# Performance work log

Hardware: AMD Instinct MI355X
Metric: run time of the kernel (lower is better)

Reference implementation:

```python
import jax, jax.numpy as jnp
import numpy as np

CK = 16          # ck_size
REP50 = 50       # extra_feature.repeat(1, 50)
BN_EPS = 1e-5
SLOPE = 0.01     # LeakyReLU default slope

def leaky(x):
    return jnp.where(x >= 0, x, SLOPE * x)

def bn(x):
    # BatchNorm1d(affine=False, track_running_stats=False): per-call batch stats
    m = jnp.mean(x, axis=0, keepdims=True)
    v = jnp.var(x, axis=0, keepdims=True)
    return (x - m) * jax.lax.rsqrt(v + BN_EPS)

def rev_within(x, lengths):
    # reverse each sequence within its valid length, keep padding in place
    B, T, _ = x.shape
    t = jnp.arange(T)[None, :]
    idx = jnp.where(t < lengths[:, None], lengths[:, None] - 1 - t, t)
    return jnp.take_along_axis(x, idx[:, :, None], axis=1)

def lstm(x, lengths, Wih, Whh, bih, bhh):
    # masked unidirectional LSTM; padded steps output zeros (pad_packed behavior)
    B, T, D = x.shape
    H = Whh.shape[1]
    xg = jnp.einsum('btd,gd->btg', x, Wih) + bih + bhh             # [B,T,4H]
    mask = (jnp.arange(T)[None, :] < lengths[:, None])[..., None]  # [B,T,1]
    def step(carry, inp):
        h, c = carry
        g, m = inp
        g = g + h @ Whh.T
        i, f, gg, o = jnp.split(g, 4, axis=-1)  # torch gate order i,f,g,o
        c_new = jax.nn.sigmoid(f) * c + jax.nn.sigmoid(i) * jnp.tanh(gg)
        h_new = jax.nn.sigmoid(o) * jnp.tanh(c_new)
        h = jnp.where(m, h_new, h)
        c = jnp.where(m, c_new, c)
        return (h, c), h_new * m
    init = (jnp.zeros((B, H), x.dtype), jnp.zeros((B, H), x.dtype))
    _, outs = jax.lax.scan(step, init, (xg.transpose(1, 0, 2), mask.transpose(1, 0, 2)))
    return outs.transpose(1, 0, 2)  # [B,T,H]

def att_var(inputs, lengths, s1_w, s1_b, s2_w):
    # NOTE: faithful to source softmax_by_length, which (due to the original
    # code) normalizes the *raw* masked logits linearly; exp() is discarded.
    B, T, D = inputs.shape
    utt = leaky(bn(inputs.reshape(-1, D) @ s1_w.T + s1_b))
    alpha = (utt @ s2_w.T).reshape(B, T)
    m = (jnp.arange(T)[None, :] < lengths[:, None]).astype(alpha.dtype)
    am = alpha * m
    alpha_ = am / (jnp.sum(am, axis=1, keepdims=True) + 1e-9)
    return jnp.einsum('bt,btd->bd', alpha_, inputs)

def item_att(x, y):
    # x: [D], y: [N, D] -> [N, 3D+1]
    xb = jnp.broadcast_to(x, y.shape)
    dist = jnp.linalg.norm(xb - y, axis=-1, keepdims=True)
    return jnp.concatenate([xb, y, dist, xb * y], axis=-1)


def setup_inputs() -> dict:
    key = jax.random.key(0)
    ks = jax.random.split(key, 30)
    D, T, B = 1024, 128, 256
    Ne, Nc, P = 64, 128, 50
    Hh = D // 2
    f32 = jnp.float32
    def rn(k, shape, s=0.05):
        return jax.random.normal(k, shape, f32) * s
    inp = {}
    inp['word_encode'] = jax.random.normal(ks[0], (B, T, D), f32)
    inp['pos_encode'] = jax.random.normal(ks[1], (Ne, Nc // CK, P), f32)
    inp['dis_encode'] = jax.random.normal(ks[2], (Ne, Nc, P), f32)
    sl = jax.random.randint(ks[3], (B,), T // 2, T + 1)
    inp['sen_lengths'] = sl.at[0].set(T)
    inp['label3'] = jax.random.randint(ks[4], (Ne, 3), -1, Nc)
    inp['emo_idx'] = jnp.arange(Ne)
    inp['cau_idx'] = jnp.arange(Ne, Ne + Nc)
    # BiLSTM params (torch layout: [4H, in])
    inp['Wih_f'] = rn(ks[5], (4 * Hh, D)); inp['Whh_f'] = rn(ks[6], (4 * Hh, Hh))
    inp['bih_f'] = rn(ks[7], (4 * Hh,));  inp['bhh_f'] = rn(ks[8], (4 * Hh,))
    inp['Wih_b'] = rn(ks[9], (4 * Hh, D)); inp['Whh_b'] = rn(ks[10], (4 * Hh, Hh))
    inp['bih_b'] = rn(ks[11], (4 * Hh,)); inp['bhh_b'] = rn(ks[12], (4 * Hh,))
    # attention / projection params
    inp['s1_w'] = rn(ks[13], (D, D)); inp['s1_b'] = rn(ks[14], (D,))
    inp['s2_w'] = rn(ks[15], (1, D))
    inp['W2_w'] = rn(ks[16], (D, 3 * D + 1 + P)); inp['W2_b'] = rn(ks[17], (D,))
    inp['Wo_w'] = rn(ks[18], (2, D)); inp['Wo_b'] = rn(ks[19], (2,))
    inp['W3_w'] = rn(ks[20], (D, 3 * D + 51 + P)); inp['W3_b'] = rn(ks[21], (D,))
    inp['cls_w'] = rn(ks[22], (2, D)); inp['cls_b'] = rn(ks[23], (2,))
    return inp


def reference(word_encode, pos_encode, dis_encode,
              Wih_f, Whh_f, bih_f, bhh_f, Wih_b, Whh_b, bih_b, bhh_b,
              s1_w, s1_b, s2_w, W2_w, W2_b, Wo_w, Wo_b, W3_w, W3_b, cls_w, cls_b,
              sen_lengths, label3, emo_idx, cau_idx):
    lengths = sen_lengths
    out_f = lstm(word_encode, lengths, Wih_f, Whh_f, bih_f, bhh_f)
    out_b = rev_within(lstm(rev_within(word_encode, lengths), lengths,
                            Wih_b, Whh_b, bih_b, bhh_b), lengths)
    Hseq = jnp.concatenate([out_f, out_b], axis=-1)          # [B,T,D]
    U = att_var(Hseq, lengths, s1_w, s1_b, s2_w)             # [B,D]
    text_emo = U[emo_idx]                                    # [Ne,D]
    text_cau = U[cau_idx]                                    # [Nc,D]
    Nc, D = text_cau.shape
    Ne = text_emo.shape[0]
    cau_chunks = text_cau.reshape(Nc // CK, CK, D)           # [Nck,CK,D]

    # ground-truth cause labels per emotion (label3 -> binary over cau utts)
    valid = (label3 >= 0)
    safe = jnp.where(valid, label3, 0)
    L = jnp.zeros((Ne, Nc), U.dtype).at[jnp.arange(Ne)[:, None], safe].max(valid.astype(U.dtype))

    def per_emo(emo, pos_j, dis_j):
        # phase-2: chunk-level attention + classification
        sc = jax.nn.softmax(jnp.einsum('d,ncd->nc', emo, cau_chunks), axis=1)
        chunkEmb = jnp.einsum('nc,ncd->nd', sc, cau_chunks)          # [Nck,D]
        delta = jnp.concatenate([item_att(emo, chunkEmb), pos_j], -1)
        hidden = leaky(bn(delta @ W2_w.T + W2_b))
        out2 = jax.nn.log_softmax(hidden @ Wo_w.T + Wo_b, axis=-1)   # [Nck,2]
        # phase-3: utterance-level with chunk prediction as extra feature
        extra = jnp.repeat(jnp.argmax(out2, axis=-1).astype(emo.dtype), CK)[:, None]
        delta_ = jnp.concatenate([item_att(emo, text_cau), dis_j,
                                  jnp.tile(extra, (1, REP50))], -1)
        h = leaky(bn(delta_ @ W3_w.T + W3_b))
        p = jax.nn.log_softmax(h @ cls_w.T + cls_b, axis=-1)         # [Nc,2]
        return out2, p

    phase2, p3 = jax.vmap(per_emo)(text_emo, pos_encode, dis_encode)
    return phase2, p3, L
```

## Files before the change

kernel.cpp:

```cpp
#include <hip/hip_runtime.h>
#include <math.h>

#define DD    1024
#define TT    128
#define BB    256
#define NE    64
#define NCC   128
#define PPP   50
#define NCK   8
#define HH    512
#define G4    2048
#define NROWS 32768
#define K3PAD 3200
#define CHUNK 8

#define F_HSEQ  0ull
#define F_XG    33554432ull
#define F_WIH   41943040ull
#define F_WHH   46137344ull
#define F_S1    48234496ull
#define F_W2    49283072ull
#define F_W3    52559872ull
#define F_BIASC 56885248ull
#define F_HST   56889344ull
#define F_CST   57413632ull
#define F_CS    57675776ull
#define F_CSQ   57676800ull
#define F_BNM   57677824ull
#define F_BNI   57678848ull
#define F_ALPHA 57679872ull
#define F_U     57712640ull
#define F_H2    57974784ull
#define F_BN2M  58499072ull
#define F_BN2I  58564608ull
#define F_EXTRA 58630144ull
#define F_BN3M  58631168ull
#define F_BN3I  58696704ull

#define F_D2    F_HSEQ
#define F_CHE   (F_HSEQ + 26214400ull)
#define F_D3    F_HSEQ
#define F_H3    F_XG

typedef short s8v __attribute__((ext_vector_type(8)));
typedef float f4v __attribute__((ext_vector_type(4)));

__device__ __forceinline__ float leakyf(float x) { return x >= 0.f ? x : 0.01f * x; }
__device__ __forceinline__ float sigmf(float x)  { return 1.f / (1.f + __expf(-x)); }

__device__ __forceinline__ float blk_sum(float v, float* s4) {
  for (int o = 32; o > 0; o >>= 1) v += __shfl_down(v, o);
  __syncthreads();
  if ((threadIdx.x & 63) == 0) s4[threadIdx.x >> 6] = v;
  __syncthreads();
  return s4[0] + s4[1] + s4[2] + s4[3];
}

__device__ __forceinline__ void cvt2(float x0, float x1, unsigned& hi, unsigned& lo) {
  unsigned b0 = __float_as_uint(x0), b1 = __float_as_uint(x1);
  hi = (b0 >> 16) | (b1 & 0xffff0000u);
  float h0 = __uint_as_float(b0 & 0xffff0000u);
  float h1 = __uint_as_float(b1 & 0xffff0000u);
  unsigned l0 = __float_as_uint(x0 - h0);
  unsigned l1 = __float_as_uint(x1 - h1);
  lo = (l0 >> 16) | (l1 & 0xffff0000u);
}

__global__ __launch_bounds__(256) void k_cvt(const float* __restrict__ src,
                                             unsigned short* __restrict__ hi,
                                             unsigned short* __restrict__ lo,
                                             int Ks, int Kd) {
  int n = blockIdx.x;
  for (int k = threadIdx.x; k < Kd; k += 256) {
    float v = (k < Ks) ? src[(size_t)n * Ks + k] : 0.f;
    unsigned b = __float_as_uint(v);
    float h = __uint_as_float(b & 0xffff0000u);
    hi[(size_t)n * Kd + k] = (unsigned short)(b >> 16);
    lo[(size_t)n * Kd + k] = (unsigned short)(__float_as_uint(v - h) >> 16);
  }
}

__global__ __launch_bounds__(256) void k_biasc(const float* __restrict__ bf1, const float* __restrict__ bf2,
                                               const float* __restrict__ bb1, const float* __restrict__ bb2,
                                               float* __restrict__ out) {
  int i = blockIdx.x * 256 + threadIdx.x;
  if (i < G4) out[i] = bf1[i] + bf2[i];
  else        out[i] = bb1[i - G4] + bb2[i - G4];
}

template <int MODE>
__global__ __launch_bounds__(256, 2) void k_mf(
    const float* __restrict__ A,
    const unsigned short* __restrict__ Ahi, const unsigned short* __restrict__ Alo,
    const unsigned short* __restrict__ Bhi, const unsigned short* __restrict__ Blo,
    const float* __restrict__ bias, float* __restrict__ C, int M, int N, int K,
    const int* __restrict__ lens, int c,
    const float* __restrict__ bnm, const float* __restrict__ bni,
    const float* __restrict__ s2w, float* __restrict__ cs,
    float* __restrict__ csq, float* __restrict__ alpha) {
  __shared__ unsigned short Ah[128][40];
  __shared__ unsigned short Al[128][40];
  __shared__ unsigned short Bh[128][40];
  __shared__ unsigned short Bl[128][40];
  const int tid = threadIdx.x;
  const int m0 = blockIdx.x * 128;
  const int n0 = blockIdx.y * 128;
  const int dir = (MODE == 3) ? blockIdx.z : 0;

  const int sr = tid >> 1;
  const int sh = tid & 1;
  const float* arow = nullptr;
  const unsigned short* ahrow = nullptr;
  const unsigned short* alrow = nullptr;
  if (MODE == 3) {
    int tl = m0 >> 8;
    int b = (m0 & 255) + sr;
    int t = c * CHUNK + tl;
    int len = lens[b];
    int r = (dir == 0) ? t : ((t < len) ? (len - 1 - t) : t);
    arow = A + ((size_t)b * TT + r) * DD;
  } else if (MODE == 0) {
    arow = A + (size_t)(m0 + sr) * K;
  } else {
    ahrow = Ahi + (size_t)(m0 + sr) * K;
    alrow = Alo + (size_t)(m0 + sr) * K;
  }
  const unsigned short* bhrow = Bhi + ((size_t)dir * N + n0 + sr) * K;
  const unsigned short* blrow = Blo + ((size_t)dir * N + n0 + sr) * K;

  const int wave = tid >> 6, lane = tid & 63;
  const int wm = wave & 1, wn = wave >> 1;
  const int quad = lane >> 4, l15 = lane & 15;

  f4v acc[4][4];
#pragma unroll
  for (int i = 0; i < 4; ++i)
#pragma unroll
    for (int j = 0; j < 4; ++j) acc[i][j] = (f4v){0.f, 0.f, 0.f, 0.f};

#pragma unroll 1
  for (int k0 = 0; k0 < K; k0 += 32) {
    __syncthreads();
    if (MODE == 1 || MODE == 2) {
      const uint4* ph = (const uint4*)(ahrow + k0 + sh * 16);
      uint4* dh = (uint4*)&Ah[sr][sh * 16];
      dh[0] = ph[0]; dh[1] = ph[1];
      const uint4* pl = (const uint4*)(alrow + k0 + sh * 16);
      uint4* dl = (uint4*)&Al[sr][sh * 16];
      dl[0] = pl[0]; dl[1] = pl[1];
    } else {
      const float4* pa = (const float4*)(arow + k0 + sh * 16);
      float4 v0 = pa[0], v1 = pa[1], v2 = pa[2], v3 = pa[3];
      unsigned h[8], l[8];
      cvt2(v0.x, v0.y, h[0], l[0]); cvt2(v0.z, v0.w, h[1], l[1]);
      cvt2(v1.x, v1.y, h[2], l[2]); cvt2(v1.z, v1.w, h[3], l[3]);
      cvt2(v2.x, v2.y, h[4], l[4]); cvt2(v2.z, v2.w, h[5], l[5]);
      cvt2(v3.x, v3.y, h[6], l[6]); cvt2(v3.z, v3.w, h[7], l[7]);
      uint4* dh = (uint4*)&Ah[sr][sh * 16];
      dh[0] = make_uint4(h[0], h[1], h[2], h[3]);
      dh[1] = make_uint4(h[4], h[5], h[6], h[7]);
      uint4* dl = (uint4*)&Al[sr][sh * 16];
      dl[0] = make_uint4(l[0], l[1], l[2], l[3]);
      dl[1] = make_uint4(l[4], l[5], l[6], l[7]);
    }
    {
      const uint4* pbh = (const uint4*)(bhrow + k0 + sh * 16);
      uint4* dbh = (uint4*)&Bh[sr][sh * 16];
      dbh[0] = pbh[0]; dbh[1] = pbh[1];
      const uint4* pbl = (const uint4*)(blrow + k0 + sh * 16);
      uint4* dbl = (uint4*)&Bl[sr][sh * 16];
      dbl[0] = pbl[0]; dbl[1] = pbl[1];
    }
    __syncthreads();
    s8v ah[4], al[4], bh[4], bl[4];
#pragma unroll
    for (int mi = 0; mi < 4; ++mi) {
      ah[mi] = *(const s8v*)&Ah[wm * 64 + mi * 16 + l15][quad * 8];
      al[mi] = *(const s8v*)&Al[wm * 64 + mi * 16 + l15][quad * 8];
    }
#pragma unroll
    for (int ni = 0; ni < 4; ++ni) {
      bh[ni] = *(const s8v*)&Bh[wn * 64 + ni * 16 + l15][quad * 8];
      bl[ni] = *(const s8v*)&Bl[wn * 64 + ni * 16 + l15][quad * 8];
    }
#pragma unroll
    for (int mi = 0; mi < 4; ++mi)
#pragma unroll
      for (int ni = 0; ni < 4; ++ni) {
        acc[mi][ni] = __builtin_amdgcn_mfma_f32_16x16x32_bf16(ah[mi], bh[ni], acc[mi][ni], 0, 0, 0);
        acc[mi][ni] = __builtin_amdgcn_mfma_f32_16x16x32_bf16(al[mi], bh[ni], acc[mi][ni], 0, 0, 0);
        acc[mi][ni] = __builtin_amdgcn_mfma_f32_16x16x32_bf16(ah[mi], bl[ni], acc[mi][ni], 0, 0, 0);
      }
  }

  const int rb = wm * 64;
  if (MODE == 0 || MODE == 3) {
    float* Cb;
    const float* bp = bias;
    if (MODE == 3) {
      int tl = m0 >> 8;
      Cb = C + (((size_t)dir * CHUNK + tl) * 256 + (m0 & 255)) * (size_t)N;
      bp = bias + (size_t)dir * N;
    } else {
      Cb = C + (size_t)m0 * N;
    }
#pragma unroll
    for (int mi = 0; mi < 4; ++mi)
#pragma unroll
      for (int ni = 0; ni < 4; ++ni) {
        int col = n0 + wn * 64 + ni * 16 + l15;
        float bv = bp[col];
#pragma unroll
        for (int r = 0; r < 4; ++r) {
          int row = rb + mi * 16 + quad * 4 + r;
          Cb[(size_t)row * N + col] = acc[mi][ni][r] + bv;
        }
      }
  } else if (MODE == 1) {
#pragma unroll
    for (int ni = 0; ni < 4; ++ni) {
      int col = n0 + wn * 64 + ni * 16 + l15;
      float bv = bias[col];
      float s = 0.f, q = 0.f;
#pragma unroll
      for (int mi = 0; mi < 4; ++mi)
#pragma unroll
        for (int r = 0; r < 4; ++r) {
          float z = acc[mi][ni][r] + bv;
          s += z;
          q += z * z;
        }
      s += __shfl_xor(s, 16); s += __shfl_xor(s, 32);
      q += __shfl_xor(q, 16); q += __shfl_xor(q, 32);
      if (quad == 0) {
        atomicAdd(&cs[col], s);
        atomicAdd(&csq[col], q);
      }
    }
  } else {
#pragma unroll
    for (int mi = 0; mi < 4; ++mi) {
      float rv[4] = {0.f, 0.f, 0.f, 0.f};
#pragma unroll
      for (int ni = 0; ni < 4; ++ni) {
        int col = n0 + wn * 64 + ni * 16 + l15;
        float bv = bias[col], mc = bnm[col], ic = bni[col], wc = s2w[col];
#pragma unroll
        for (int r = 0; r < 4; ++r) {
          float z = acc[mi][ni][r] + bv;
          rv[r] += leakyf((z - mc) * ic) * wc;
        }
      }
#pragma unroll
      for (int r = 0; r < 4; ++r) {
        float v = rv[r];
        v += __shfl_xor(v, 1); v += __shfl_xor(v, 2);
        v += __shfl_xor(v, 4); v += __shfl_xor(v, 8);
        if (l15 == 0) atomicAdd(&alpha[m0 + rb + mi * 16 + quad * 4 + r], v);
      }
    }
  }
}

__global__ __launch_bounds__(256, 2) void k_rec(
    const unsigned short* __restrict__ Bhi, const unsigned short* __restrict__ Blo,
    const float* __restrict__ XG, const int* __restrict__ lens,
    const float* __restrict__ Hcur, float* __restrict__ Hnext,
    float* __restrict__ Cst,
    unsigned short* __restrict__ Hhi, unsigned short* __restrict__ Hlo, int t) {
  __shared__ unsigned short Ah[64][40];
  __shared__ unsigned short Al[64][40];
  __shared__ unsigned short Bh[64][40];
  __shared__ unsigned short Bl[64][40];
  const int tid = threadIdx.x;
  const int b0 = blockIdx.x * 64;
  const int j0 = blockIdx.y * 16;
  const int dir = blockIdx.z;
  const int tl = t & (CHUNK - 1);
  const int srow = tid >> 2;
  const int skq = (tid & 3) * 8;
  const int bg = srow >> 4, bjj = srow & 15;
  const float* arow = Hcur + ((size_t)dir * BB + b0 + srow) * HH;
  const unsigned short* bhrow = Bhi + ((size_t)dir * G4 + bg * HH + j0 + bjj) * HH;
  const unsigned short* blrow = Blo + ((size_t)dir * G4 + bg * HH + j0 + bjj) * HH;
  const int wave = tid >> 6, lane = tid & 63;
  const int quad = lane >> 4, l15 = lane & 15;

  f4v acc[4];
#pragma unroll
  for (int g = 0; g < 4; ++g) acc[g] = (f4v){0.f, 0.f, 0.f, 0.f};

#pragma unroll 1
  for (int k0 = 0; k0 < HH; k0 += 32) {
    __syncthreads();
    {
      const float4* pa = (const float4*)(arow + k0 + skq);
      float4 v0 = pa[0], v1 = pa[1];
      unsigned h[4], l[4];
      cvt2(v0.x, v0.y, h[0], l[0]); cvt2(v0.z, v0.w, h[1], l[1]);
      cvt2(v1.x, v1.y, h[2], l[2]); cvt2(v1.z, v1.w, h[3], l[3]);
      *(uint4*)&Ah[srow][skq] = make_uint4(h[0], h[1], h[2], h[3]);
      *(uint4*)&Al[srow][skq] = make_uint4(l[0], l[1], l[2], l[3]);
      *(uint4*)&Bh[srow][skq] = *(const uint4*)(bhrow + k0 + skq);
      *(uint4*)&Bl[srow][skq] = *(const uint4*)(blrow + k0 + skq);
    }
    __syncthreads();
    s8v ah = *(const s8v*)&Ah[wave * 16 + l15][quad * 8];
    s8v al = *(const s8v*)&Al[wave * 16 + l15][quad * 8];
#pragma unroll
    for (int g = 0; g < 4; ++g) {
      s8v bh = *(const s8v*)&Bh[g * 16 + l15][quad * 8];
      s8v bl = *(const s8v*)&Bl[g * 16 + l15][quad * 8];
      acc[g] = __builtin_amdgcn_mfma_f32_16x16x32_bf16(ah, bh, acc[g], 0, 0, 0);
      acc[g] = __builtin_amdgcn_mfma_f32_16x16x32_bf16(al, bh, acc[g], 0, 0, 0);
      acc[g] = __builtin_amdgcn_mfma_f32_16x16x32_bf16(ah, bl, acc[g], 0, 0, 0);
    }
  }

  const int j = j0 + l15;
#pragma unroll
  for (int r = 0; r < 4; ++r) {
    int b = b0 + wave * 16 + quad * 4 + r;
    int len = lens[b];
    bool m = t < len;
    size_t xgb = (((size_t)dir * CHUNK + tl) * BB + b) * G4 + j;
    float gi = acc[0][r] + XG[xgb];
    float gf = acc[1][r] + XG[xgb + HH];
    float gg = acc[2][r] + XG[xgb + 2 * HH];
    float go = acc[3][r] + XG[xgb + 3 * HH];
    size_t sidx = ((size_t)dir * BB + b) * HH + j;
    float c_old = Cst[sidx];
    float cn = sigmf(gf) * c_old + sigmf(gi) * tanhf(gg);
    float hn = sigmf(go) * tanhf(cn);
    if (m) {
      Cst[sidx] = cn;
      Hnext[sidx] = hn;
      int ro = dir ? (len - 1 - t) : t;
      size_t hidx = ((size_t)b * TT + ro) * DD + dir * HH + j;
      unsigned hb = __float_as_uint(hn);
      Hhi[hidx] = (unsigned short)(hb >> 16);
      Hlo[hidx] = (unsigned short)(__float_as_uint(hn - __uint_as_float(hb & 0xffff0000u)) >> 16);
    } else {
      Hnext[sidx] = Hcur[sidx];
    }
  }
}

__global__ __launch_bounds__(256) void k_bnfinal(const float* __restrict__ cs, const float* __restrict__ csq,
                                                 float* __restrict__ bnm, float* __restrict__ bni, float invN) {
  int i = blockIdx.x * 256 + threadIdx.x;
  if (i < DD) {
    float m = cs[i] * invN;
    float v = csq[i] * invN - m * m;
    bnm[i] = m;
    bni[i] = rsqrtf(v + 1e-5f);
  }
}

__global__ __launch_bounds__(128) void k_asum(float* __restrict__ alpha, const int* __restrict__ lens) {
  int b = blockIdx.x;
  int t = threadIdx.x;
  int len = lens[b];
  float v = (t < len) ? alpha[b * TT + t] : 0.f;
  float s = v;
  for (int o = 32; o > 0; o >>= 1) s += __shfl_down(s, o);
  __shared__ float sw[2];
  if ((t & 63) == 0) sw[t >> 6] = s;
  __syncthreads();
  float S = sw[0] + sw[1] + 1e-9f;
  alpha[b * TT + t] = v / S;
}

__global__ __launch_bounds__(256) void k_U(const unsigned short* __restrict__ Hhi,
                                           const unsigned short* __restrict__ Hlo,
                                           const float* __restrict__ alpha,
                                           float* __restrict__ U) {
  int b = blockIdx.x;
  int tid = threadIdx.x;
  __shared__ float al[TT];
  if (tid < TT) al[tid] = alpha[b * TT + tid];
  __syncthreads();
  float4 s = make_float4(0.f, 0.f, 0.f, 0.f);
  size_t base = (size_t)b * TT * DD + tid * 4;
#pragma unroll 4
  for (int t = 0; t < TT; ++t) {
    float a = al[t];
    ushort4 hv = *(const ushort4*)(Hhi + base + (size_t)t * DD);
    ushort4 lv = *(const ushort4*)(Hlo + base + (size_t)t * DD);
    s.x += a * (__uint_as_float((unsigned)hv.x << 16) + __uint_as_float((unsigned)lv.x << 16));
    s.y += a * (__uint_as_float((unsigned)hv.y << 16) + __uint_as_float((unsigned)lv.y << 16));
    s.z += a * (__uint_as_float((unsigned)hv.z << 16) + __uint_as_float((unsigned)lv.z << 16));
    s.w += a * (__uint_as_float((unsigned)hv.w << 16) + __uint_as_float((unsigned)lv.w << 16));
  }
  *(float4*)(U + (size_t)b * DD + tid * 4) = s;
}

__global__ __launch_bounds__(256) void k_p2a(const float* __restrict__ U,
                                             const int* __restrict__ emoI,
                                             const int* __restrict__ cauI,
                                             float* __restrict__ chunkEmb) {
  int e = blockIdx.x;
  int tid = threadIdx.x;
  __shared__ float emoS[DD];
  __shared__ float sc[NCK][16];
  const float* Ue = U + (size_t)emoI[e] * DD;
  for (int i = tid; i < DD; i += 256) emoS[i] = Ue[i];
  __syncthreads();
  int w = tid >> 6, lane = tid & 63;
  for (int p = w; p < 128; p += 4) {
    const float* y = U + (size_t)cauI[p] * DD;
    float s = 0;
    for (int d = lane; d < DD; d += 64) s += emoS[d] * y[d];
    for (int o = 32; o > 0; o >>= 1) s += __shfl_down(s, o);
    if (lane == 0) sc[p >> 4][p & 15] = s;
  }
  __syncthreads();
  if (tid < NCK) {
    float mx = -1e30f;
    for (int c = 0; c < 16; ++c) mx = fmaxf(mx, sc[tid][c]);
    float sum = 0;
    for (int c = 0; c < 16; ++c) {
      float ev = __expf(sc[tid][c] - mx);
      sc[tid][c] = ev;
      sum += ev;
    }
    float inv = 1.f / sum;
    for (int c = 0; c < 16; ++c) sc[tid][c] *= inv;
  }
  __syncthreads();
  int d = tid * 4;
  for (int nn = 0; nn < NCK; ++nn) {
    float4 s = make_float4(0.f, 0.f, 0.f, 0.f);
    for (int c = 0; c < 16; ++c) {
      float wc = sc[nn][c];
      float4 y = *(const float4*)(U + (size_t)cauI[nn * 16 + c] * DD + d);
      s.x += wc * y.x; s.y += wc * y.y; s.z += wc * y.z; s.w += wc * y.w;
    }
    *(float4*)(chunkEmb + ((size_t)e * NCK + nn) * DD + d) = s;
  }
}

__global__ __launch_bounds__(256) void k_delta2(const float* __restrict__ U,
                                                const int* __restrict__ emoI,
                                                const float* __restrict__ chunkEmb,
                                                const float* __restrict__ pos,
                                                float* __restrict__ delta2) {
  int e = blockIdx.x >> 3, nn = blockIdx.x & 7;
  int tid = threadIdx.x;
  const float* emo = U + (size_t)emoI[e] * DD;
  const float* y = chunkEmb + ((size_t)e * NCK + nn) * DD;
  __shared__ float s4[4];
  float ds = 0;
  for (int d = tid; d < DD; d += 256) {
    float df = emo[d] - y[d];
    ds += df * df;
  }
  float dist = sqrtf(blk_sum(ds, s4));
  float* out = delta2 + ((size_t)e * NCK + nn) * K3PAD;
  for (int c = tid; c < K3PAD; c += 256) {
    float v;
    if (c < 1024) v = emo[c];
    else if (c < 2048) v = y[c - 1024];
    else if (c == 2048) v = dist;
    else if (c < 3073) { int d = c - 2049; v = emo[d] * y[d]; }
    else if (c < 3123) v = pos[((size_t)e * NCK + nn) * PPP + (c - 3073)];
    else v = 0.f;
    out[c] = v;
  }
}

__global__ __launch_bounds__(256) void k_bnstats(const float* __restrict__ X,
                                                 float* __restrict__ bm, float* __restrict__ bi, int R) {
  int gid = blockIdx.x * 256 + threadIdx.x;
  int e = gid >> 10, col = gid & 1023;
  const float* p = X + (size_t)e * R * DD + col;
  float s = 0, s2 = 0;
  for (int r = 0; r < R; ++r) {
    float v = p[(size_t)r * DD];
    s += v;
    s2 += v * v;
  }
  float m = s / R;
  float var = s2 / R - m * m;
  bm[gid] = m;
  bi[gid] = rsqrtf(var + 1e-5f);
}

__global__ __launch_bounds__(256) void k_out2(const float* __restrict__ h2,
                                              const float* __restrict__ bm, const float* __restrict__ bi,
                                              const float* __restrict__ Wo, const float* __restrict__ Wob,
                                              float* __restrict__ out, float* __restrict__ extraf) {
  int e = blockIdx.x >> 3, nn = blockIdx.x & 7;
  int tid = threadIdx.x;
  const float* row = h2 + ((size_t)e * NCK + nn) * DD;
  float l0 = 0, l1 = 0;
  for (int col = tid; col < DD; col += 256) {
    float h = leakyf((row[col] - bm[e * DD + col]) * bi[e * DD + col]);
    l0 += h * Wo[col];
    l1 += h * Wo[DD + col];
  }
  __shared__ float s4[4];
  l0 = blk_sum(l0, s4);
  l1 = blk_sum(l1, s4);
  if (tid == 0) {
    l0 += Wob[0];
    l1 += Wob[1];
    float mx = fmaxf(l0, l1);
    float lse = mx + logf(__expf(l0 - mx) + __expf(l1 - mx));
    out[((size_t)e * NCK + nn) * 2 + 0] = l0 - lse;
    out[((size_t)e * NCK + nn) * 2 + 1] = l1 - lse;
    extraf[e * NCK + nn] = (l1 > l0) ? 1.f : 0.f;
  }
}

__global__ __launch_bounds__(256) void k_delta3(const float* __restrict__ U,
                                                const int* __restrict__ emoI,
                                                const int* __restrict__ cauI,
                                                const float* __restrict__ dis,
                                                const float* __restrict__ extraf,
                                                float* __restrict__ delta3) {
  int e = blockIdx.x >> 7, c = blockIdx.x & 127;
  int tid = threadIdx.x;
  const float* emo = U + (size_t)emoI[e] * DD;
  const float* y = U + (size_t)cauI[c] * DD;
  __shared__ float s4[4];
  float ds = 0;
  for (int d = tid; d < DD; d += 256) {
    float df = emo[d] - y[d];
    ds += df * df;
  }
  float dist = sqrtf(blk_sum(ds, s4));
  float ex = extraf[e * NCK + (c >> 4)];
  float* out = delta3 + ((size_t)e * NCC + c) * K3PAD;
  for (int col = tid; col < K3PAD; col += 256) {
    float v;
    if (col < 1024) v = emo[col];
    else if (col < 2048) v = y[col - 1024];
    else if (col == 2048) v = dist;
    else if (col < 3073) { int d = col - 2049; v = emo[d] * y[d]; }
    else if (col < 3123) v = dis[((size_t)e * NCC + c) * PPP + (col - 3073)];
    else if (col < 3173) v = ex;
    else v = 0.f;
    out[col] = v;
  }
}

__global__ __launch_bounds__(256) void k_p3(const float* __restrict__ h3,
                                            const float* __restrict__ bm, const float* __restrict__ bi,
                                            const float* __restrict__ cw, const float* __restrict__ cb,
                                            float* __restrict__ out) {
  int e = blockIdx.x >> 7, c = blockIdx.x & 127;
  int tid = threadIdx.x;
  const float* row = h3 + ((size_t)e * NCC + c) * DD;
  float l0 = 0, l1 = 0;
  for (int col = tid; col < DD; col += 256) {
    float h = leakyf((row[col] - bm[e * DD + col]) * bi[e * DD + col]);
    l0 += h * cw[col];
    l1 += h * cw[DD + col];
  }
  __shared__ float s4[4];
  l0 = blk_sum(l0, s4);
  l1 = blk_sum(l1, s4);
  if (tid == 0) {
    l0 += cb[0];
    l1 += cb[1];
    float mx = fmaxf(l0, l1);
    float lse = mx + logf(__expf(l0 - mx) + __expf(l1 - mx));
    out[((size_t)e * NCC + c) * 2 + 0] = l0 - lse;
    out[((size_t)e * NCC + c) * 2 + 1] = l1 - lse;
  }
}

__global__ __launch_bounds__(256) void k_L(const int* __restrict__ lab, float* __restrict__ out) {
  int i = blockIdx.x * 256 + threadIdx.x;
  int e = i >> 7, c = i & 127;
  int a = lab[e * 3 + 0], b = lab[e * 3 + 1], d = lab[e * 3 + 2];
  out[i] = (a == c || b == c || d == c) ? 1.f : 0.f;
}

extern "C" void kernel_launch(void* const* d_in, const int* in_sizes, int n_in,
                              void* d_out, int out_size, void* d_ws, size_t ws_size,
                              hipStream_t stream) {
  (void)in_sizes; (void)n_in; (void)out_size; (void)ws_size;
  const float* X     = (const float*)d_in[0];
  const float* pos   = (const float*)d_in[1];
  const float* dis   = (const float*)d_in[2];
  const int*   lens  = (const int*)d_in[3];
  const int*   lab3  = (const int*)d_in[4];
  const int*   emoI  = (const int*)d_in[5];
  const int*   cauI  = (const int*)d_in[6];
  const float* Wih_f = (const float*)d_in[7];
  const float* Whh_f = (const float*)d_in[8];
  const float* bih_f = (const float*)d_in[9];
  const float* bhh_f = (const float*)d_in[10];
  const float* Wih_b = (const float*)d_in[11];
  const float* Whh_b = (const float*)d_in[12];
  const float* bih_b = (const float*)d_in[13];
  const float* bhh_b = (const float*)d_in[14];
  const float* s1w   = (const float*)d_in[15];
  const float* s1b   = (const float*)d_in[16];
  const float* s2w   = (const float*)d_in[17];
  const float* W2w   = (const float*)d_in[18];
  const float* W2b   = (const float*)d_in[19];
  const float* Wow   = (const float*)d_in[20];
  const float* Wob   = (const float*)d_in[21];
  const float* W3w   = (const float*)d_in[22];
  const float* W3b   = (const float*)d_in[23];
  const float* clsw  = (const float*)d_in[24];
  const float* clsb  = (const float*)d_in[25];
  float* ws = (float*)d_ws;
  float* out = (float*)d_out;

  unsigned short* Hhi = (unsigned short*)(ws + F_HSEQ);
  unsigned short* Hlo = Hhi + (size_t)NROWS * DD;
  unsigned short* WIHhi = (unsigned short*)(ws + F_WIH);
  unsigned short* WIHlo = WIHhi + (size_t)2 * 2048 * 1024;
  unsigned short* WHHhi = (unsigned short*)(ws + F_WHH);
  unsigned short* WHHlo = WHHhi + (size_t)2 * 2048 * 512;
  unsigned short* S1hi  = (unsigned short*)(ws + F_S1);
  unsigned short* S1lo  = S1hi + (size_t)1024 * 1024;
  unsigned short* W2hi  = (unsigned short*)(ws + F_W2);
  unsigned short* W2lo  = W2hi + (size_t)1024 * K3PAD;
  unsigned short* W3hi  = (unsigned short*)(ws + F_W3);
  unsigned short* W3lo  = W3hi + (size_t)1024 * K3PAD;

  hipMemsetAsync(ws + F_HSEQ, 0, (size_t)33554432 * sizeof(float), stream);
  hipMemsetAsync(ws + F_HST, 0, (size_t)(524288 + 262144) * sizeof(float), stream);
  hipMemsetAsync(ws + F_CS, 0, (size_t)2048 * sizeof(float), stream);
  hipMemsetAsync(ws + F_ALPHA, 0, (size_t)32768 * sizeof(float), stream);

  k_cvt<<<2048, 256, 0, stream>>>(Wih_f, WIHhi, WIHlo, 1024, 1024);
  k_cvt<<<2048, 256, 0, stream>>>(Wih_b, WIHhi + (size_t)2048 * 1024, WIHlo + (size_t)2048 * 1024, 1024, 1024);
  k_cvt<<<2048, 256, 0, stream>>>(Whh_f, WHHhi, WHHlo, 512, 512);
  k_cvt<<<2048, 256, 0, stream>>>(Whh_b, WHHhi + (size_t)2048 * 512, WHHlo + (size_t)2048 * 512, 512, 512);
  k_cvt<<<1024, 256, 0, stream>>>(s1w, S1hi, S1lo, 1024, 1024);
  k_cvt<<<1024, 256, 0, stream>>>(W2w, W2hi, W2lo, 3123, K3PAD);
  k_cvt<<<1024, 256, 0, stream>>>(W3w, W3hi, W3lo, 3173, K3PAD);
  k_biasc<<<16, 256, 0, stream>>>(bih_f, bhh_f, bih_b, bhh_b, ws + F_BIASC);

  for (int c = 0; c < TT / CHUNK; ++c) {
    k_mf<3><<<dim3(16, 16, 2), 256, 0, stream>>>(X, nullptr, nullptr, WIHhi, WIHlo,
                                                 ws + F_BIASC, ws + F_XG,
                                                 2048, 2048, 1024, lens, c,
                                                 nullptr, nullptr, nullptr, nullptr, nullptr, nullptr);
    for (int tt = 0; tt < CHUNK; ++tt) {
      int t = c * CHUNK + tt;
      const float* Hcur = ws + F_HST + (size_t)(t & 1) * 262144;
      float* Hnext = ws + F_HST + (size_t)((t + 1) & 1) * 262144;
      k_rec<<<dim3(4, 32, 2), 256, 0, stream>>>(WHHhi, WHHlo, ws + F_XG, lens,
                                                Hcur, Hnext, ws + F_CST, Hhi, Hlo, t);
    }
  }

  k_mf<1><<<dim3(256, 8), 256, 0, stream>>>(nullptr, Hhi, Hlo, S1hi, S1lo, s1b, nullptr,
                                            NROWS, 1024, 1024, nullptr, 0,
                                            nullptr, nullptr, nullptr,
                                            ws + F_CS, ws + F_CSQ, nullptr);
  k_bnfinal<<<4, 256, 0, stream>>>(ws + F_CS, ws + F_CSQ, ws + F_BNM, ws + F_BNI, 1.f / NROWS);
  k_mf<2><<<dim3(256, 8), 256, 0, stream>>>(nullptr, Hhi, Hlo, S1hi, S1lo, s1b, nullptr,
                                            NROWS, 1024, 1024, nullptr, 0,
                                            ws + F_BNM, ws + F_BNI, s2w,
                                            nullptr, nullptr, ws + F_ALPHA);
  k_asum<<<BB, TT, 0, stream>>>(ws + F_ALPHA, lens);
  k_U<<<BB, 256, 0, stream>>>(Hhi, Hlo, ws + F_ALPHA, ws + F_U);

  k_p2a<<<NE, 256, 0, stream>>>(ws + F_U, emoI, cauI, ws + F_CHE);
  k_delta2<<<NE * NCK, 256, 0, stream>>>(ws + F_U, emoI, ws + F_CHE, pos, ws + F_D2);
  k_mf<0><<<dim3(4, 8), 256, 0, stream>>>(ws + F_D2, nullptr, nullptr, W2hi, W2lo, W2b, ws + F_H2,
                                          512, 1024, K3PAD, nullptr, 0,
                                          nullptr, nullptr, nullptr, nullptr, nullptr, nullptr);
  k_bnstats<<<256, 256, 0, stream>>>(ws + F_H2, ws + F_BN2M, ws + F_BN2I, NCK);
  k_out2<<<NE * NCK, 256, 0, stream>>>(ws + F_H2, ws + F_BN2M, ws + F_BN2I, Wow, Wob,
                                       out, ws + F_EXTRA);

  k_delta3<<<NE * NCC, 256, 0, stream>>>(ws + F_U, emoI, cauI, dis, ws + F_EXTRA, ws + F_D3);
  k_mf<0><<<dim3(64, 8), 256, 0, stream>>>(ws + F_D3, nullptr, nullptr, W3hi, W3lo, W3b, ws + F_H3,
                                           8192, 1024, K3PAD, nullptr, 0,
                                           nullptr, nullptr, nullptr, nullptr, nullptr, nullptr);
  k_bnstats<<<256, 256, 0, stream>>>(ws + F_H3, ws + F_BN3M, ws + F_BN3I, NCC);
  k_p3<<<NE * NCC, 256, 0, stream>>>(ws + F_H3, ws + F_BN3M, ws + F_BN3I, clsw, clsb, out + 1024);
  k_L<<<32, 256, 0, stream>>>(lab3, out + 17408);
}
```

Before: 4.740 ms.

## Fuse eight LSTM recurrence steps into one persistent kernel with inter-block flags

Replaces the per-timestep recurrent kernel launches with one launch per chunk of eight steps. Each block keeps its slice of the recurrent weights resident in swizzled shared memory and keeps its cell state in registers. Blocks that share a batch tile and direction synchronise through global atomic counters between steps. The hidden state is exchanged as pre-split bf16 hi/lo halves rather than fp32, and tanh is replaced by an exp-based form. This removes launch overhead and repeated weight reloads. In exchange it relies on all 256 blocks being co-resident to avoid deadlock, and the fast tanh may lose a little precision.

```diff
diff --git a/kernel.cpp b/kernel.cpp
--- a/kernel.cpp
+++ b/kernel.cpp
@@ -41,12 +41,17 @@
 #define F_CHE   (F_HSEQ + 26214400ull)
 #define F_D3    F_HSEQ
 #define F_H3    F_XG
+#define F_SYNC  F_H2
 
 typedef short s8v __attribute__((ext_vector_type(8)));
 typedef float f4v __attribute__((ext_vector_type(4)));
 
 __device__ __forceinline__ float leakyf(float x) { return x >= 0.f ? x : 0.01f * x; }
 __device__ __forceinline__ float sigmf(float x)  { return 1.f / (1.f + __expf(-x)); }
+__device__ __forceinline__ float tanhfast(float x) {
+  float e = __expf(2.f * x);
+  return 1.f - 2.f / (e + 1.f);
+}
 
 __device__ __forceinline__ float blk_sum(float v, float* s4) {
   for (int o = 32; o > 0; o >>= 1) v += __shfl_down(v, o);
@@ -262,88 +267,143 @@
   }
 }
 
-__global__ __launch_bounds__(256, 2) void k_rec(
+__global__ __launch_bounds__(256, 1) void k_rec8(
     const unsigned short* __restrict__ Bhi, const unsigned short* __restrict__ Blo,
     const float* __restrict__ XG, const int* __restrict__ lens,
-    const float* __restrict__ Hcur, float* __restrict__ Hnext,
+    unsigned short* __restrict__ Hsh, unsigned short* __restrict__ Hsl,
     float* __restrict__ Cst,
-    unsigned short* __restrict__ Hhi, unsigned short* __restrict__ Hlo, int t) {
-  __shared__ unsigned short Ah[64][40];
-  __shared__ unsigned short Al[64][40];
-  __shared__ unsigned short Bh[64][40];
-  __shared__ unsigned short Bl[64][40];
+    unsigned short* __restrict__ Hhi, unsigned short* __restrict__ Hlo,
+    int* __restrict__ syncc, int c) {
+  __shared__ unsigned short Bsh[64 * 512];
+  __shared__ unsigned short Bsl[64 * 512];
   const int tid = threadIdx.x;
   const int b0 = blockIdx.x * 64;
   const int j0 = blockIdx.y * 16;
   const int dir = blockIdx.z;
-  const int tl = t & (CHUNK - 1);
-  const int srow = tid >> 2;
-  const int skq = (tid & 3) * 8;
-  const int bg = srow >> 4, bjj = srow & 15;
-  const float* arow = Hcur + ((size_t)dir * BB + b0 + srow) * HH;
-  const unsigned short* bhrow = Bhi + ((size_t)dir * G4 + bg * HH + j0 + bjj) * HH;
-  const unsigned short* blrow = Blo + ((size_t)dir * G4 + bg * HH + j0 + bjj) * HH;
+  const int grp = blockIdx.x * 2 + dir;
+
+  for (int i = tid; i < 64 * 64; i += 256) {
+    int row = i >> 6, s = i & 63;
+    int sp = s ^ (row & 7);
+    int grow = dir * G4 + (row >> 4) * HH + j0 + (row & 15);
+    ((uint4*)Bsh)[row * 64 + sp] = ((const uint4*)(Bhi + (size_t)grow * HH))[s];
+    ((uint4*)Bsl)[row * 64 + sp] = ((const uint4*)(Blo + (size_t)grow * HH))[s];
+  }
+
   const int wave = tid >> 6, lane = tid & 63;
   const int quad = lane >> 4, l15 = lane & 15;
-
-  f4v acc[4];
-#pragma unroll
-  for (int g = 0; g < 4; ++g) acc[g] = (f4v){0.f, 0.f, 0.f, 0.f};
-
-#pragma unroll 1
-  for (int k0 = 0; k0 < HH; k0 += 32) {
-    __syncthreads();
-    {
-      const float4* pa = (const float4*)(arow + k0 + skq);
-      float4 v0 = pa[0], v1 = pa[1];
-      unsigned h[4], l[4];
-      cvt2(v0.x, v0.y, h[0], l[0]); cvt2(v0.z, v0.w, h[1], l[1]);
-      cvt2(v1.x, v1.y, h[2], l[2]); cvt2(v1.z, v1.w, h[3], l[3]);
-      *(uint4*)&Ah[srow][skq] = make_uint4(h[0], h[1], h[2], h[3]);
-      *(uint4*)&Al[srow][skq] = make_uint4(l[0], l[1], l[2], l[3]);
-      *(uint4*)&Bh[srow][skq] = *(const uint4*)(bhrow + k0 + skq);
-      *(uint4*)&Bl[srow][skq] = *(const uint4*)(blrow + k0 + skq);
-    }
-    __syncthreads();
-    s8v ah = *(const s8v*)&Ah[wave * 16 + l15][quad * 8];
-    s8v al = *(const s8v*)&Al[wave * 16 + l15][quad * 8];
-#pragma unroll
-    for (int g = 0; g < 4; ++g) {
-      s8v bh = *(const s8v*)&Bh[g * 16 + l15][quad * 8];
-      s8v bl = *(const s8v*)&Bl[g * 16 + l15][quad * 8];
-      acc[g] = __builtin_amdgcn_mfma_f32_16x16x32_bf16(ah, bh, acc[g], 0, 0, 0);
-      acc[g] = __builtin_amdgcn_mfma_f32_16x16x32_bf16(al, bh, acc[g], 0, 0, 0);
-      acc[g] = __builtin_amdgcn_mfma_f32_16x16x32_bf16(ah, bl, acc[g], 0, 0, 0);
-    }
-  }
-
   const int j = j0 + l15;
+  const int amrow = b0 + wave * 16 + l15;
+
+  int bv[4], lenv[4];
+  size_t sidx[4];
+  float cstate[4];
+  unsigned short hhr[4], hlr[4];
 #pragma unroll
   for (int r = 0; r < 4; ++r) {
-    int b = b0 + wave * 16 + quad * 4 + r;
-    int len = lens[b];
-    bool m = t < len;
-    size_t xgb = (((size_t)dir * CHUNK + tl) * BB + b) * G4 + j;
-    float gi = acc[0][r] + XG[xgb];
-    float gf = acc[1][r] + XG[xgb + HH];
-    float gg = acc[2][r] + XG[xgb + 2 * HH];
-    float go = acc[3][r] + XG[xgb + 3 * HH];
-    size_t sidx = ((size_t)dir * BB + b) * HH + j;
-    float c_old = Cst[sidx];
-    float cn = sigmf(gf) * c_old + sigmf(gi) * tanhf(gg);
-    float hn = sigmf(go) * tanhf(cn);
-    if (m) {
-      Cst[sidx] = cn;
-      Hnext[sidx] = hn;
-      int ro = dir ? (len - 1 - t) : t;
-      size_t hidx = ((size_t)b * TT + ro) * DD + dir * HH + j;
-      unsigned hb = __float_as_uint(hn);
-      Hhi[hidx] = (unsigned short)(hb >> 16);
-      Hlo[hidx] = (unsigned short)(__float_as_uint(hn - __uint_as_float(hb & 0xffff0000u)) >> 16);
-    } else {
-      Hnext[sidx] = Hcur[sidx];
-    }
-  }
+    bv[r] = b0 + wave * 16 + quad * 4 + r;
+    lenv[r] = lens[bv[r]];
+    sidx[r] = ((size_t)dir * BB + bv[r]) * HH + j;
+    cstate[r] = Cst[sidx[r]];
+  }
+  {
+    size_t pbase = ((size_t)dir * BB) * HH;
+#pragma unroll
+    for (int r = 0; r < 4; ++r) {
+      size_t idx = pbase + (size_t)bv[r] * HH + j;
+      hhr[r] = Hsh[idx];
+      hlr[r] = Hsl[idx];
+    }
+  }
+  __syncthreads();
+
+  for (int tt = 0; tt < CHUNK; ++tt) {
+    const int t = c * CHUNK + tt;
+    const int rpar = t & 1, wpar = (t + 1) & 1;
+
+    if (tt > 0) {
+      if (tid == 0) {
+        while (__hip_atomic_load(syncc + (size_t)(t - 1) * 8 + grp,
+                                 __ATOMIC_RELAXED, __HIP_MEMORY_SCOPE_AGENT) < 32) {
+          __builtin_amdgcn_s_sleep(1);
+        }
+        __threadfence();
+      }
+      __syncthreads();
+    }
+
+    float xgv[4][4];
+#pragma unroll
+    for (int r = 0; r < 4; ++r) {
+      size_t xgb = (((size_t)dir * CHUNK + tt) * BB + bv[r]) * (size_t)G4 + j;
+#pragma unroll
+      for (int g = 0; g < 4; ++g) xgv[r][g] = XG[xgb + (size_t)g * HH];
+    }
+
+    const unsigned short* arh = Hsh + (((size_t)rpar * 2 + dir) * BB + amrow) * HH;
+    const unsigned short* arl = Hsl + (((size_t)rpar * 2 + dir) * BB + amrow) * HH;
+
+    f4v acc[4];
+#pragma unroll
+    for (int g = 0; g < 4; ++g) acc[g] = (f4v){0.f, 0.f, 0.f, 0.f};
+
+#pragma unroll
+    for (int ks = 0; ks < 16; ++ks) {
+      uint4 ch = *(const uint4*)(arh + ks * 32 + quad * 8);
+      uint4 cl = *(const uint4*)(arl + ks * 32 + quad * 8);
+      s8v ah = *(s8v*)&ch;
+      s8v al = *(s8v*)&cl;
+#pragma unroll
+      for (int g = 0; g < 4; ++g) {
+        int row = g * 16 + l15;
+        int sp = (ks * 4 + quad) ^ (l15 & 7);
+        s8v bh = *(const s8v*)(Bsh + row * 512 + sp * 8);
+        s8v bl = *(const s8v*)(Bsl + row * 512 + sp * 8);
+        acc[g] = __builtin_amdgcn_mfma_f32_16x16x32_bf16(ah, bh, acc[g], 0, 0, 0);
+        acc[g] = __builtin_amdgcn_mfma_f32_16x16x32_bf16(al, bh, acc[g], 0, 0, 0);
+        acc[g] = __builtin_amdgcn_mfma_f32_16x16x32_bf16(ah, bl, acc[g], 0, 0, 0);
+      }
+    }
+
+    size_t wbase = (((size_t)wpar * 2 + dir) * BB) * HH;
+#pragma unroll
+    for (int r = 0; r < 4; ++r) {
+      if (t < lenv[r]) {
+        float gi = acc[0][r] + xgv[r][0];
+        float gf = acc[1][r] + xgv[r][1];
+        float gg = acc[2][r] + xgv[r][2];
+        float go = acc[3][r] + xgv[r][3];
+        float cn = sigmf(gf) * cstate[r] + sigmf(gi) * tanhfast(gg);
+        float hn = sigmf(go) * tanhfast(cn);
+        cstate[r] = cn;
+        unsigned hb = __float_as_uint(hn);
+        unsigned short h16 = (unsigned short)(hb >> 16);
+        unsigned short l16 =
+            (unsigned short)(__float_as_uint(hn - __uint_as_float(hb & 0xffff0000u)) >> 16);
+        hhr[r] = h16;
+        hlr[r] = l16;
+        int ro = dir ? (lenv[r] - 1 - t) : t;
+        size_t hidx = ((size_t)bv[r] * TT + ro) * DD + (size_t)dir * HH + j;
+        Hhi[hidx] = h16;
+        Hlo[hidx] = l16;
+      }
+      size_t wi = wbase + (size_t)bv[r] * HH + j;
+      Hsh[wi] = hhr[r];
+      Hsl[wi] = hlr[r];
+    }
+
+    if (tt < CHUNK - 1) {
+      __syncthreads();
+      if (tid == 0) {
+        __threadfence();
+        __hip_atomic_fetch_add(syncc + (size_t)t * 8 + grp, 1,
+                               __ATOMIC_RELAXED, __HIP_MEMORY_SCOPE_AGENT);
+      }
+    }
+  }
+
+#pragma unroll
+  for (int r = 0; r < 4; ++r) Cst[sidx[r]] = cstate[r];
 }
 
 __global__ __launch_bounds__(256) void k_bnfinal(const float* __restrict__ cs, const float* __restrict__ csq,
@@ -623,11 +683,14 @@
   unsigned short* W2lo  = W2hi + (size_t)1024 * K3PAD;
   unsigned short* W3hi  = (unsigned short*)(ws + F_W3);
   unsigned short* W3lo  = W3hi + (size_t)1024 * K3PAD;
+  unsigned short* Hsh   = (unsigned short*)(ws + F_HST);
+  unsigned short* Hsl   = Hsh + (size_t)2 * 2 * BB * HH;
 
   hipMemsetAsync(ws + F_HSEQ, 0, (size_t)33554432 * sizeof(float), stream);
   hipMemsetAsync(ws + F_HST, 0, (size_t)(524288 + 262144) * sizeof(float), stream);
   hipMemsetAsync(ws + F_CS, 0, (size_t)2048 * sizeof(float), stream);
   hipMemsetAsync(ws + F_ALPHA, 0, (size_t)32768 * sizeof(float), stream);
+  hipMemsetAsync(ws + F_SYNC, 0, 4096, stream);
 
   k_cvt<<<2048, 256, 0, stream>>>(Wih_f, WIHhi, WIHlo, 1024, 1024);
   k_cvt<<<2048, 256, 0, stream>>>(Wih_b, WIHhi + (size_t)2048 * 1024, WIHlo + (size_t)2048 * 1024, 1024, 1024);
@@ -643,13 +706,9 @@
                                                  ws + F_BIASC, ws + F_XG,
                                                  2048, 2048, 1024, lens, c,
                                                  nullptr, nullptr, nullptr, nullptr, nullptr, nullptr);
-    for (int tt = 0; tt < CHUNK; ++tt) {
-      int t = c * CHUNK + tt;
-      const float* Hcur = ws + F_HST + (size_t)(t & 1) * 262144;
-      float* Hnext = ws + F_HST + (size_t)((t + 1) & 1) * 262144;
-      k_rec<<<dim3(4, 32, 2), 256, 0, stream>>>(WHHhi, WHHlo, ws + F_XG, lens,
-                                                Hcur, Hnext, ws + F_CST, Hhi, Hlo, t);
-    }
+    k_rec8<<<dim3(4, 32, 2), 256, 0, stream>>>(WHHhi, WHHlo, ws + F_XG, lens,
+                                               Hsh, Hsl, ws + F_CST, Hhi, Hlo,
+                                               (int*)(ws + F_SYNC), c);
   }
 
   k_mf<1><<<dim3(256, 8), 256, 0, stream>>>(nullptr, Hhi, Hlo, S1hi, S1lo, s1b, nullptr,
```

Measured after the change: 5.344 ms. 1.13x slower.
